# Kernel tuning notes

Measured on AMD Instinct MI355X. Metric: run time of the kernel, lower is better.

## Reference

```python
import jax, jax.numpy as jnp
import numpy as np
from jax import lax

B, T, N, CIN, CH, COUT, K, KS, E = 2, 16, 2048, 32, 64, 64, 3, 3, 32768


def setup_inputs() -> dict:
    key = jax.random.key(0)
    ks = jax.random.split(key, 20)
    s = 0.05
    p = lambda k, shp: s * jax.random.normal(k, shp, dtype=jnp.float32)
    return {
        "X": jax.random.normal(ks[0], (B, T, N, CIN), dtype=jnp.float32),
        "edge_index": jax.random.randint(ks[1], (2, E), 0, N),
        "edge_weight": jax.random.uniform(ks[2], (E,), dtype=jnp.float32),
        "tc1_w1": p(ks[3], (CH, CIN, 1, KS)), "tc1_b1": p(ks[4], (CH,)),
        "tc1_w2": p(ks[5], (CH, CIN, 1, KS)), "tc1_b2": p(ks[6], (CH,)),
        "tc1_w3": p(ks[7], (CH, CIN, 1, KS)), "tc1_b3": p(ks[8], (CH,)),
        "cheb_w": p(ks[9], (K, CH, CH)), "cheb_b": p(ks[10], (CH,)),
        "tc2_w1": p(ks[11], (COUT, CH, 1, KS)), "tc2_b1": p(ks[12], (COUT,)),
        "tc2_w2": p(ks[13], (COUT, CH, 1, KS)), "tc2_b2": p(ks[14], (COUT,)),
        "tc2_w3": p(ks[15], (COUT, CH, 1, KS)), "tc2_b3": p(ks[16], (COUT,)),
        "bn_gamma": jnp.ones((N,), jnp.float32),
        "bn_beta": jnp.zeros((N,), jnp.float32),
    }


def _tconv(X, w1, b1, w2, b2, w3, b3):
    # X: (B, T, N, C) -> (B, C, N, T), gated temporal conv over last axis
    x = jnp.transpose(X, (0, 3, 2, 1))
    dn = ("NCHW", "OIHW", "NCHW")
    c = lambda w, b: lax.conv_general_dilated(x, w, (1, 1), "VALID", dimension_numbers=dn) + b[None, :, None, None]
    out = jax.nn.relu(c(w1, b1) + jax.nn.sigmoid(c(w2, b2)) + c(w3, b3))
    return jnp.transpose(out, (0, 3, 2, 1))


def _cheb(x, edge_index, edge_weight, W, b):
    # ChebConv, sym normalization, lambda_max=2 -> L_hat = -D^{-1/2} A D^{-1/2}
    row, col = edge_index[0], edge_index[1]
    w = jnp.where(row == col, 0.0, edge_weight)  # get_laplacian removes self-loops
    deg = jax.ops.segment_sum(w, row, num_segments=N)
    safe = jnp.where(deg > 0, deg, 1.0)
    dis = jnp.where(deg > 0, lax.rsqrt(safe), 0.0)
    norm = -dis[row] * w * dis[col]  # (E,)

    def prop(z):  # z: (B, T, N, C)
        zm = jnp.moveaxis(z, 2, 0)                      # (N, B, T, C)
        msg = zm[col] * norm[:, None, None, None]       # (E, B, T, C)
        agg = jax.ops.segment_sum(msg, row, num_segments=N)
        return jnp.moveaxis(agg, 0, 2)

    Tx0 = x
    out = jnp.einsum("btnc,co->btno", Tx0, W[0])
    Tx1 = prop(Tx0)
    out = out + jnp.einsum("btnc,co->btno", Tx1, W[1])
    for k in range(2, K):
        Tx2 = 2.0 * prop(Tx1) - Tx0
        out = out + jnp.einsum("btnc,co->btno", Tx2, W[k])
        Tx0, Tx1 = Tx1, Tx2
    return out + b


def reference(X, edge_index, edge_weight, tc1_w1, tc1_b1, tc1_w2, tc1_b2, tc1_w3, tc1_b3,
              cheb_w, cheb_b, tc2_w1, tc2_b1, tc2_w2, tc2_b2, tc2_w3, tc2_b3,
              bn_gamma, bn_beta):
    t1 = _tconv(X, tc1_w1, tc1_b1, tc1_w2, tc1_b2, tc1_w3, tc1_b3)   # (B, T-2, N, CH)
    t2 = jax.nn.relu(_cheb(t1, edge_index, edge_weight, cheb_w, cheb_b))
    t3 = _tconv(t2, tc2_w1, tc2_b1, tc2_w2, tc2_b2, tc2_w3, tc2_b3)  # (B, T-4, N, COUT)
    t = jnp.transpose(t3, (0, 2, 1, 3))  # (B, N, T', COUT): N is BN channel axis
    mu = jnp.mean(t, axis=(0, 2, 3), keepdims=True)
    var = jnp.var(t, axis=(0, 2, 3), keepdims=True)
    t = (t - mu) * lax.rsqrt(var + 1e-5) * bn_gamma[None, :, None, None] + bn_beta[None, :, None, None]
    return jnp.transpose(t, (0, 2, 1, 3))
```

## Files before the change

### kernel.cpp

```cpp
#include <hip/hip_runtime.h>
#include <cstdint>
#include <cstddef>

typedef unsigned short ushort_t;
typedef short bf16x8 __attribute__((ext_vector_type(8)));
typedef float f32x4 __attribute__((ext_vector_type(4)));

#define N_NODES 2048
#define E_EDGES 32768

constexpr int OFS_X     = 0;
constexpr int OFS_EW    = 2097152;
constexpr int OFS_SMALL = 2129920;
constexpr int SMALL_TOTAL = 72128;
constexpr int OFS_T1W1 = 2129920;
constexpr int OFS_T1B1 = 2136064;
constexpr int OFS_T1W2 = 2136128;
constexpr int OFS_T1B2 = 2142272;
constexpr int OFS_T1W3 = 2142336;
constexpr int OFS_T1B3 = 2148480;
constexpr int OFS_CHW  = 2148544;
constexpr int OFS_CHB  = 2160832;
constexpr int OFS_T2W1 = 2160896;
constexpr int OFS_T2B1 = 2173184;
constexpr int OFS_T2W2 = 2173248;
constexpr int OFS_T2B2 = 2185536;
constexpr int OFS_T2W3 = 2185600;
constexpr int OFS_T2B3 = 2197888;
constexpr int OFS_GAM  = 2197952;
constexpr int OFS_BET  = 2200000;
constexpr int CAN_TOTAL = 2202048;

__device__ __align__(16) ushort_t g_t1b [3670016];
__device__ __align__(16) ushort_t g_tx1b[3670016];
__device__ __align__(16) ushort_t g_tx2b[3670016];
__device__ __align__(16) ushort_t g_t2b [3670016];
__device__ __align__(16) float    g_t3 [3145728];
__device__ float    g_deg[N_NODES];
__device__ int      g_cnt[N_NODES];
__device__ int      g_cur[N_NODES];
__device__ float    g_scale[N_NODES];
__device__ float    g_shift[N_NODES];
__device__ __align__(8) int2 g_csrp[E_EDGES];
__device__ int      g_rowstart[N_NODES + 1];
__device__ __align__(16) ushort_t g_can[CAN_TOTAL];
__device__ __align__(16) ushort_t g_wb1[18432];
__device__ __align__(16) ushort_t g_wb2[36864];
__device__ __align__(16) ushort_t g_wbc[12288];

__device__ __forceinline__ float bfu(ushort_t u) { return __uint_as_float(((unsigned)u) << 16); }
__device__ __forceinline__ ushort_t f2bf(float f) {
    unsigned u = __float_as_uint(f);
    u = u + 0x7fffu + ((u >> 16) & 1u);
    return (ushort_t)(u >> 16);
}
#define BF16_ONES_PAIR 0x3F803F80u

__global__ void convert_big_kernel(const void* __restrict__ X, const void* __restrict__ ew,
                                   const unsigned* __restrict__ gam) {
    int idx = blockIdx.x * 256 + threadIdx.x;
    bool isbf = (gam[0] == BF16_ONES_PAIR);
    if (idx < N_NODES) { g_deg[idx] = 0.f; g_cnt[idx] = 0; g_cur[idx] = 0; }
    if (idx < 2097152) {
        g_can[idx] = isbf ? ((const ushort_t*)X)[idx] : f2bf(((const float*)X)[idx]);
    } else {
        int i = idx - 2097152;
        g_can[idx] = isbf ? ((const ushort_t*)ew)[i] : f2bf(((const float*)ew)[i]);
    }
}

struct SmallPtrs { const void* p[16]; };

__global__ void convert_small_kernel(SmallPtrs sp, const unsigned* __restrict__ gam) {
    const int sizes[16] = {6144, 64, 6144, 64, 6144, 64, 12288, 64,
                           12288, 64, 12288, 64, 12288, 64, 2048, 2048};
    int idx = blockIdx.x * 256 + threadIdx.x;
    if (idx >= SMALL_TOTAL) return;
    bool isbf = (gam[0] == BF16_ONES_PAIR);
    int j = 0, local = idx;
    while (local >= sizes[j]) { local -= sizes[j]; ++j; }
    const void* p = sp.p[j];
    g_can[OFS_SMALL + idx] = isbf ? ((const ushort_t*)p)[local]
                                  : f2bf(((const float*)p)[local]);
}

__global__ void repack_kernel() {
    int idx = blockIdx.x * 256 + threadIdx.x;
    if (idx < 18432) {
        int j = idx & 7, lane = (idx >> 3) & 63, kk = (idx >> 9) % 3;
        int nt = (idx / 1536) & 3, set = idx / 6144;
        int o = nt * 16 + (lane & 15);
        int k = kk * 32 + (lane >> 4) * 8 + j;
        int ci = k & 31, ks = k >> 5;
        int base = (set == 0) ? OFS_T1W1 : (set == 1) ? OFS_T1W2 : OFS_T1W3;
        g_wb1[idx] = g_can[base + o * 96 + ci * 3 + ks];
    } else if (idx < 18432 + 36864) {
        int t = idx - 18432;
        int j = t & 7, lane = (t >> 3) & 63, kk = (t >> 9) % 6;
        int nt = (t / 3072) & 3, set = t / 12288;
        int o = nt * 16 + (lane & 15);
        int k = kk * 32 + (lane >> 4) * 8 + j;
        int ci = k & 63, ks = k >> 6;
        int base = (set == 0) ? OFS_T2W1 : (set == 1) ? OFS_T2W2 : OFS_T2W3;
        g_wb2[t] = g_can[base + o * 192 + ci * 3 + ks];
    } else {
        int t = idx - 18432 - 36864;
        int j = t & 7, lane = (t >> 3) & 63, kk = (t >> 9) % 6;
        int nt = t / 3072;
        int o = nt * 16 + (lane & 15);
        int k = kk * 32 + (lane >> 4) * 8 + j;
        int sec = k >> 6, c = k & 63;
        g_wbc[t] = g_can[OFS_CHW + sec * 4096 + c * 64 + o];
    }
}

__global__ void edge_count_kernel(const int* __restrict__ ei) {
    int e = blockIdx.x * 256 + threadIdx.x;
    if (e >= E_EDGES) return;
    int r = ei[e];
    int c = ei[E_EDGES + e];
    float w = (r == c) ? 0.f : bfu(g_can[OFS_EW + e]);
    atomicAdd(&g_deg[r], w);
    atomicAdd(&g_cnt[r], 1);
}

__global__ void scan_kernel() {
    __shared__ int part[256];
    __shared__ int pre[256];
    int t = threadIdx.x;
    int base = t * 8;
    int s = 0;
#pragma unroll
    for (int i = 0; i < 8; ++i) s += g_cnt[base + i];
    part[t] = s;
    __syncthreads();
    if (t == 0) {
        int a = 0;
        for (int i = 0; i < 256; ++i) { pre[i] = a; a += part[i]; }
    }
    __syncthreads();
    int a = pre[t];
#pragma unroll
    for (int i = 0; i < 8; ++i) { g_rowstart[base + i] = a; a += g_cnt[base + i]; }
    if (t == 255) g_rowstart[N_NODES] = a;
}

__global__ void edge_scatter_kernel(const int* __restrict__ ei) {
    int e = blockIdx.x * 256 + threadIdx.x;
    if (e >= E_EDGES) return;
    int r = ei[e];
    int c = ei[E_EDGES + e];
    float w = (r == c) ? 0.f : bfu(g_can[OFS_EW + e]);
    float dr = g_deg[r], dc = g_deg[c];
    float nr = dr > 0.f ? rsqrtf(dr) : 0.f;
    float nc = dc > 0.f ? rsqrtf(dc) : 0.f;
    int pos = atomicAdd(&g_cur[r], 1);
    int at = g_rowstart[r] + pos;
    g_csrp[at] = make_int2(c, __float_as_int(-nr * w * nc));
}

template <int LAYER>
__global__ __launch_bounds__(256) void tconv_mfma_kernel() {
    constexpr int CIN_  = (LAYER == 1) ? 32 : 64;
    constexpr int T_in  = (LAYER == 1) ? 16 : 14;
    constexpr int T_out = (LAYER == 1) ? 14 : 12;
    constexpr int KST   = (CIN_ * 3) / 32;
    constexpr int PADK  = (LAYER == 1) ? 104 : 200;
    constexpr int OB1 = (LAYER == 1) ? OFS_T1B1 : OFS_T2B1;
    constexpr int OB2 = (LAYER == 1) ? OFS_T1B2 : OFS_T2B2;
    constexpr int OB3 = (LAYER == 1) ? OFS_T1B3 : OFS_T2B3;

    __shared__ ushort_t xs[64 * PADK];

    const int tid = threadIdx.x;
    const int lane = tid & 63;
    const int wv = tid >> 6;
    const int m0 = blockIdx.x * 64;
    const int n0 = m0 & (N_NODES - 1);
    const int s  = m0 >> 11;
    const int b  = s / T_out;
    const int t  = s - b * T_out;

#pragma unroll
    for (int ks = 0; ks < 3; ++ks) {
        if constexpr (LAYER == 1) {
            const ushort4* src = (const ushort4*)(g_can + OFS_X +
                ((size_t)(b * T_in + t + ks) * N_NODES + n0) * 32);
            for (int i = tid; i < 512; i += 256) {
                ushort4 v = src[i];
                int row = i >> 3, c4 = i & 7;
                *(ushort4*)&xs[row * PADK + ks * 32 + c4 * 4] = v;
            }
        } else {
            const ushort4* src = (const ushort4*)(g_t2b +
                ((size_t)(b * T_in + t + ks) * N_NODES + n0) * 64);
            for (int i = tid; i < 1024; i += 256) {
                ushort4 v = src[i];
                int row = i >> 4, c4 = i & 15;
                *(ushort4*)&xs[row * PADK + ks * 64 + c4 * 4] = v;
            }
        }
    }
    __syncthreads();

    const ushort_t* WB = (LAYER == 1) ? g_wb1 : g_wb2;
    f32x4 acc[3][4];
#pragma unroll
    for (int st = 0; st < 3; ++st)
#pragma unroll
        for (int nt = 0; nt < 4; ++nt) acc[st][nt] = (f32x4){0.f, 0.f, 0.f, 0.f};

    const int arow = wv * 16 + (lane & 15);
    const int kofs = (lane >> 4) * 8;
#pragma unroll
    for (int kk = 0; kk < KST; ++kk) {
        bf16x8 av = *(const bf16x8*)&xs[arow * PADK + kk * 32 + kofs];
#pragma unroll
        for (int st = 0; st < 3; ++st)
#pragma unroll
            for (int nt = 0; nt < 4; ++nt) {
                bf16x8 bv = ((const bf16x8*)WB)[((st * 4 + nt) * KST + kk) * 64 + lane];
                acc[st][nt] = __builtin_amdgcn_mfma_f32_16x16x32_bf16(av, bv, acc[st][nt], 0, 0, 0);
            }
    }

    const int col = lane & 15;
    const int quad = lane >> 4;
#pragma unroll
    for (int nt = 0; nt < 4; ++nt) {
        int o = nt * 16 + col;
        float b1 = bfu(g_can[OB1 + o]);
        float b2 = bfu(g_can[OB2 + o]);
        float b3 = bfu(g_can[OB3 + o]);
#pragma unroll
        for (int reg = 0; reg < 4; ++reg) {
            int m = m0 + wv * 16 + quad * 4 + reg;
            float q = acc[1][nt][reg] + b2;
            float v = (acc[0][nt][reg] + b1) + 1.f / (1.f + expf(-q)) + (acc[2][nt][reg] + b3);
            v = v > 0.f ? v : 0.f;
            if constexpr (LAYER == 1) g_t1b[(size_t)m * 64 + o] = f2bf(v);
            else                      g_t3 [(size_t)m * 64 + o] = v;
        }
    }
}

template <int MODE>
__global__ __launch_bounds__(256) void prop_kernel() {
    const ushort_t* __restrict__ src = (MODE == 0) ? g_t1b : g_tx1b;
    ushort_t* __restrict__ dst = (MODE == 0) ? g_tx1b : g_tx2b;
    const int n = blockIdx.x;
    const int c = threadIdx.x & 63;
    const int sg = threadIdx.x >> 6;
    const int beg = g_rowstart[n], end = g_rowstart[n + 1];
    const int s0 = sg * 7;

    float acc[7];
#pragma unroll
    for (int j = 0; j < 7; ++j) acc[j] = 0.f;

    int e = beg;
    for (; e + 2 <= end; e += 2) {
        int2 p0 = g_csrp[e];
        int2 p1 = g_csrp[e + 1];
        float w0 = __int_as_float(p0.y);
        float w1 = __int_as_float(p1.y);
        size_t b0 = ((size_t)p0.x << 6) + c;
        size_t b1 = ((size_t)p1.x << 6) + c;
#pragma unroll
        for (int j = 0; j < 7; ++j) {
            size_t so = (size_t)(s0 + j) * (N_NODES * 64);
            float v0 = bfu(src[so + b0]);
            float v1 = bfu(src[so + b1]);
            acc[j] = fmaf(w1, v1, fmaf(w0, v0, acc[j]));
        }
    }
    if (e < end) {
        int2 p0 = g_csrp[e];
        float w0 = __int_as_float(p0.y);
        size_t b0 = ((size_t)p0.x << 6) + c;
#pragma unroll
        for (int j = 0; j < 7; ++j)
            acc[j] = fmaf(w0, bfu(src[(size_t)(s0 + j) * (N_NODES * 64) + b0]), acc[j]);
    }

#pragma unroll
    for (int j = 0; j < 7; ++j) {
        size_t off = ((size_t)(s0 + j) * N_NODES + n) * 64 + c;
        if constexpr (MODE == 0) dst[off] = f2bf(acc[j]);
        else                     dst[off] = f2bf(2.f * acc[j] - bfu(g_t1b[off]));
    }
}

__global__ __launch_bounds__(256) void cheb_mfma_kernel() {
    constexpr int PADK = 200;
    __shared__ ushort_t xs[64 * PADK];

    const int tid = threadIdx.x;
    const int lane = tid & 63;
    const int wv = tid >> 6;
    const int m0 = blockIdx.x * 64;

#pragma unroll
    for (int sec = 0; sec < 3; ++sec) {
        const ushort_t* sp = (sec == 0) ? g_t1b : (sec == 1) ? g_tx1b : g_tx2b;
        const ushort4* src = (const ushort4*)(sp + (size_t)m0 * 64);
        for (int i = tid; i < 1024; i += 256) {
            ushort4 v = src[i];
            int row = i >> 4, c4 = i & 15;
            *(ushort4*)&xs[row * PADK + sec * 64 + c4 * 4] = v;
        }
    }
    __syncthreads();

    f32x4 acc[4];
#pragma unroll
    for (int nt = 0; nt < 4; ++nt) acc[nt] = (f32x4){0.f, 0.f, 0.f, 0.f};

    const int arow = wv * 16 + (lane & 15);
    const int kofs = (lane >> 4) * 8;
#pragma unroll
    for (int kk = 0; kk < 6; ++kk) {
        bf16x8 av = *(const bf16x8*)&xs[arow * PADK + kk * 32 + kofs];
#pragma unroll
        for (int nt = 0; nt < 4; ++nt) {
            bf16x8 bv = ((const bf16x8*)g_wbc)[(nt * 6 + kk) * 64 + lane];
            acc[nt] = __builtin_amdgcn_mfma_f32_16x16x32_bf16(av, bv, acc[nt], 0, 0, 0);
        }
    }

    const int col = lane & 15;
    const int quad = lane >> 4;
#pragma unroll
    for (int nt = 0; nt < 4; ++nt) {
        int o = nt * 16 + col;
        float bias = bfu(g_can[OFS_CHB + o]);
#pragma unroll
        for (int reg = 0; reg < 4; ++reg) {
            int m = m0 + wv * 16 + quad * 4 + reg;
            float v = acc[nt][reg] + bias;
            g_t2b[(size_t)m * 64 + o] = f2bf(v > 0.f ? v : 0.f);
        }
    }
}

__global__ __launch_bounds__(256) void bn_stats_kernel() {
    int n = blockIdx.x;
    int tid = threadIdx.x;
    int c = tid & 63;
    int sg = tid >> 6;
    float s1 = 0.f, s2 = 0.f;
    for (int s = sg; s < 24; s += 4) {
        float v = g_t3[((size_t)(s * N_NODES + n)) * 64 + c];
        s1 += v;
        s2 += v * v;
    }
    __shared__ float r1[256], r2[256];
    r1[tid] = s1;
    r2[tid] = s2;
    __syncthreads();
    for (int st = 128; st > 0; st >>= 1) {
        if (tid < st) { r1[tid] += r1[tid + st]; r2[tid] += r2[tid + st]; }
        __syncthreads();
    }
    if (tid == 0) {
        const float inv = 1.f / 1536.f;
        float mean = r1[0] * inv;
        float var  = r2[0] * inv - mean * mean;
        float rstd = rsqrtf(var + 1e-5f);
        float g = bfu(g_can[OFS_GAM + n]), be = bfu(g_can[OFS_BET + n]);
        g_scale[n] = rstd * g;
        g_shift[n] = be - mean * rstd * g;
    }
}

__global__ __launch_bounds__(256) void bn_apply_kernel(void* __restrict__ outp,
                                                       const unsigned* __restrict__ gam) {
    size_t i = (size_t)blockIdx.x * 256 + threadIdx.x;
    size_t e = i * 4;
    int n = (int)((e >> 6) & (N_NODES - 1));
    float4 v = *reinterpret_cast<const float4*>(g_t3 + e);
    float sc = g_scale[n], sh = g_shift[n];
    float r0 = v.x * sc + sh;
    float r1 = v.y * sc + sh;
    float r2 = v.z * sc + sh;
    float r3 = v.w * sc + sh;
    if (gam[0] == BF16_ONES_PAIR) {
        ushort4 ov;
        ov.x = f2bf(r0); ov.y = f2bf(r1); ov.z = f2bf(r2); ov.w = f2bf(r3);
        *reinterpret_cast<ushort4*>((ushort_t*)outp + e) = ov;
    } else {
        float4 ov = make_float4(r0, r1, r2, r3);
        *reinterpret_cast<float4*>((float*)outp + e) = ov;
    }
}

extern "C" void kernel_launch(void* const* d_in, const int* in_sizes, int n_in,
                              void* d_out, int out_size, void* d_ws, size_t ws_size,
                              hipStream_t stream) {
    const int* ei = (const int*)d_in[1];
    const unsigned* gam = (const unsigned*)d_in[17];

    convert_big_kernel<<<8320, 256, 0, stream>>>(d_in[0], d_in[2], gam);
    SmallPtrs sp;
    for (int i = 0; i < 16; ++i) sp.p[i] = d_in[3 + i];
    convert_small_kernel<<<(SMALL_TOTAL + 255) / 256, 256, 0, stream>>>(sp, gam);

    edge_count_kernel<<<E_EDGES / 256, 256, 0, stream>>>(ei);
    scan_kernel<<<1, 256, 0, stream>>>();
    edge_scatter_kernel<<<E_EDGES / 256, 256, 0, stream>>>(ei);

    repack_kernel<<<264, 256, 0, stream>>>();

    tconv_mfma_kernel<1><<<896, 256, 0, stream>>>();

    prop_kernel<0><<<N_NODES, 256, 0, stream>>>();
    prop_kernel<1><<<N_NODES, 256, 0, stream>>>();
    cheb_mfma_kernel<<<896, 256, 0, stream>>>();

    tconv_mfma_kernel<2><<<768, 256, 0, stream>>>();

    bn_stats_kernel<<<N_NODES, 256, 0, stream>>>();
    bn_apply_kernel<<<3072, 256, 0, stream>>>(d_out, gam);
}
```

Measured before the change: 197.2 us.

## Fuse BatchNorm statistics into second temporal conv epilogue via atomics

Accumulates per-node sum and sum-of-squares in the layer-2 tconv epilogue using wave shuffles and global atomicAdd, removing the separate bn_stats kernel and its full re-read of t3. bn_apply now computes scale/shift per block from the accumulated sums into shared memory. This trades a kernel launch and a 12MB read for atomic contention and nondeterministic float summation order. It also relies on an n0 variable being defined in the tconv kernel.

New measurement: 225.0 us. 14.1% more time.

```diff
diff --git a/kernel.cpp b/kernel.cpp
--- a/kernel.cpp
+++ b/kernel.cpp
@@ -39,8 +39,8 @@
 __device__ float    g_deg[N_NODES];
 __device__ int      g_cnt[N_NODES];
 __device__ int      g_cur[N_NODES];
-__device__ float    g_scale[N_NODES];
-__device__ float    g_shift[N_NODES];
+__device__ float    g_bnsum[N_NODES];
+__device__ float    g_bnsumsq[N_NODES];
 __device__ __align__(8) int2 g_csrp[E_EDGES];
 __device__ int      g_rowstart[N_NODES + 1];
 __device__ __align__(16) ushort_t g_can[CAN_TOTAL];
@@ -49,6 +49,8 @@
 __device__ __align__(16) ushort_t g_wbc[12288];
 
 __device__ __forceinline__ float bfu(ushort_t u) { return __uint_as_float(((unsigned)u) << 16); }
+__device__ __forceinline__ float lo16(unsigned u) { return __uint_as_float(u << 16); }
+__device__ __forceinline__ float hi16(unsigned u) { return __uint_as_float(u & 0xffff0000u); }
 __device__ __forceinline__ ushort_t f2bf(float f) {
     unsigned u = __float_as_uint(f);
     u = u + 0x7fffu + ((u >> 16) & 1u);
@@ -60,7 +62,10 @@
                                    const unsigned* __restrict__ gam) {
     int idx = blockIdx.x * 256 + threadIdx.x;
     bool isbf = (gam[0] == BF16_ONES_PAIR);
-    if (idx < N_NODES) { g_deg[idx] = 0.f; g_cnt[idx] = 0; g_cur[idx] = 0; }
+    if (idx < N_NODES) {
+        g_deg[idx] = 0.f; g_cnt[idx] = 0; g_cur[idx] = 0;
+        g_bnsum[idx] = 0.f; g_bnsumsq[idx] = 0.f;
+    }
     if (idx < 2097152) {
         g_can[idx] = isbf ? ((const ushort_t*)X)[idx] : f2bf(((const float*)X)[idx]);
     } else {
@@ -226,6 +231,8 @@
 
     const int col = lane & 15;
     const int quad = lane >> 4;
+    float rs1[4] = {0.f, 0.f, 0.f, 0.f};
+    float rs2[4] = {0.f, 0.f, 0.f, 0.f};
 #pragma unroll
     for (int nt = 0; nt < 4; ++nt) {
         int o = nt * 16 + col;
@@ -238,8 +245,29 @@
             float q = acc[1][nt][reg] + b2;
             float v = (acc[0][nt][reg] + b1) + 1.f / (1.f + expf(-q)) + (acc[2][nt][reg] + b3);
             v = v > 0.f ? v : 0.f;
-            if constexpr (LAYER == 1) g_t1b[(size_t)m * 64 + o] = f2bf(v);
-            else                      g_t3 [(size_t)m * 64 + o] = v;
+            if constexpr (LAYER == 1) {
+                g_t1b[(size_t)m * 64 + o] = f2bf(v);
+            } else {
+                g_t3[(size_t)m * 64 + o] = v;
+                rs1[reg] += v;
+                rs2[reg] += v * v;
+            }
+        }
+    }
+    if constexpr (LAYER == 2) {
+#pragma unroll
+        for (int reg = 0; reg < 4; ++reg) {
+            float s1 = rs1[reg], s2 = rs2[reg];
+#pragma unroll
+            for (int msk = 1; msk < 16; msk <<= 1) {
+                s1 += __shfl_xor(s1, msk, 64);
+                s2 += __shfl_xor(s2, msk, 64);
+            }
+            if (col == 0) {
+                int n = n0 + wv * 16 + quad * 4 + reg;
+                atomicAdd(&g_bnsum[n], s1);
+                atomicAdd(&g_bnsumsq[n], s2);
+            }
         }
     }
 }
@@ -343,43 +371,27 @@
     }
 }
 
-__global__ __launch_bounds__(256) void bn_stats_kernel() {
-    int n = blockIdx.x;
-    int tid = threadIdx.x;
-    int c = tid & 63;
-    int sg = tid >> 6;
-    float s1 = 0.f, s2 = 0.f;
-    for (int s = sg; s < 24; s += 4) {
-        float v = g_t3[((size_t)(s * N_NODES + n)) * 64 + c];
-        s1 += v;
-        s2 += v * v;
-    }
-    __shared__ float r1[256], r2[256];
-    r1[tid] = s1;
-    r2[tid] = s2;
-    __syncthreads();
-    for (int st = 128; st > 0; st >>= 1) {
-        if (tid < st) { r1[tid] += r1[tid + st]; r2[tid] += r2[tid + st]; }
-        __syncthreads();
-    }
-    if (tid == 0) {
+__global__ __launch_bounds__(256) void bn_apply_kernel(void* __restrict__ outp,
+                                                       const unsigned* __restrict__ gam) {
+    __shared__ float ssc[16], ssh[16];
+    const int bid = blockIdx.x;
+    const int tid = threadIdx.x;
+    const int n0 = (bid * 16) & (N_NODES - 1);
+    if (tid < 16) {
+        int n = n0 + tid;
         const float inv = 1.f / 1536.f;
-        float mean = r1[0] * inv;
-        float var  = r2[0] * inv - mean * mean;
+        float mean = g_bnsum[n] * inv;
+        float var  = g_bnsumsq[n] * inv - mean * mean;
         float rstd = rsqrtf(var + 1e-5f);
         float g = bfu(g_can[OFS_GAM + n]), be = bfu(g_can[OFS_BET + n]);
-        g_scale[n] = rstd * g;
-        g_shift[n] = be - mean * rstd * g;
-    }
-}
-
-__global__ __launch_bounds__(256) void bn_apply_kernel(void* __restrict__ outp,
-                                                       const unsigned* __restrict__ gam) {
-    size_t i = (size_t)blockIdx.x * 256 + threadIdx.x;
-    size_t e = i * 4;
-    int n = (int)((e >> 6) & (N_NODES - 1));
+        ssc[tid] = rstd * g;
+        ssh[tid] = be - mean * rstd * g;
+    }
+    __syncthreads();
+    size_t e = ((size_t)bid * 256 + tid) * 4;
+    int nloc = tid >> 4;
     float4 v = *reinterpret_cast<const float4*>(g_t3 + e);
-    float sc = g_scale[n], sh = g_shift[n];
+    float sc = ssc[nloc], sh = ssh[nloc];
     float r0 = v.x * sc + sh;
     float r1 = v.y * sc + sh;
     float r2 = v.z * sc + sh;
@@ -419,6 +431,5 @@
 
     tconv_mfma_kernel<2><<<768, 256, 0, stream>>>();
 
-    bn_stats_kernel<<<N_NODES, 256, 0, stream>>>();
     bn_apply_kernel<<<3072, 256, 0, stream>>>(d_out, gam);
 }
```
